# Kernel tuning notes

Hardware: AMD Instinct MI355X
Metric: run time of the kernel (lower is better)

## Reference

```python
import jax, jax.numpy as jnp
import numpy as np

T = 2_000_000  # timesteps


def setup_inputs() -> dict:
    key = jax.random.key(0)
    u = jax.random.normal(key, (T, 2), dtype=jnp.float32) * 10.0  # external forces per step
    x0 = jnp.zeros((4,), dtype=jnp.float32)  # [z1, v1, z2, v2]
    c = jnp.array([10.0, 10.0, 10.0], dtype=jnp.float32)   # trainable damping c1,c2,c3
    m = jnp.array([20.0, 10.0], dtype=jnp.float32)          # masses m1,m2 (frozen)
    k = jnp.array([2.0e3, 1.0e3, 5.0e3], dtype=jnp.float32) # stiffness k1,k2,k3 (frozen)
    dt = jnp.float32(0.002)
    return {"u": u, "x0": x0, "c": c, "m": m, "k": k, "dt": dt}


def reference(u, x0, c, m, k, dt):
    c1, c2, c3 = c[0], c[1], c[2]
    m1, m2 = m[0], m[1]
    k1, k2, k3 = k[0], k[1], k[2]

    def deriv(x, ut):
        # x = [z1, v1, z2, v2]; returns dx/dt = [v1, a1, v2, a2]
        z1, v1, z2, v2 = x[0], x[1], x[2], x[3]
        a1 = (ut[0] - (c1 + c2) * v1 + c2 * v2 - (k1 + k2) * z1 + k2 * z2) / m1
        a2 = (ut[1] - (c3 + c2) * v2 + c2 * v1 - (k3 + k2) * z2 + k2 * z1) / m2
        return jnp.stack([v1, a1, v2, a2])

    half = dt * 0.5

    def step(x, ut):
        s1 = deriv(x, ut)
        s2 = deriv(x + half * s1, ut)
        s3 = deriv(x + half * s2, ut)
        s4 = deriv(x + dt * s3, ut)
        xn = x + (dt / 6.0) * (s1 + 2.0 * s2 + 2.0 * s3 + s4)
        y = jnp.stack([xn[0], xn[2]])  # positions z1, z2 (matches cell output)
        return xn, y

    _, ys = jax.lax.scan(step, x0, u)
    return ys  # [T, 2]
```

## Files before the change

### kernel.cpp

```cpp
#include <hip/hip_runtime.h>

#define BLK 256
#define LS  32
#define SPB (BLK*LS)
#define STR (LS+1)

#define WC_M   0
#define WC_N   16
#define WC_SK  24
#define WC_GK  152
#define WC_TOT 280

#define WS_BAR_F32   1024
#define BAR_ARR_U32  0
#define BAR_FLAG_U32 272
#define BAR_BYTES    1152

typedef unsigned long long u64t;
union F2U { float2 f; u64t u; };

#define STEP4(Mx,Nx, s0,s1,s2,s3, ux,uy, n0,n1,n2,n3)                                              \
  n0 = fmaf(Mx[0],s0,  fmaf(Mx[1],s1,  fmaf(Mx[2],s2,  fmaf(Mx[3],s3,  fmaf(Nx[0],ux, Nx[1]*uy))))); \
  n1 = fmaf(Mx[4],s0,  fmaf(Mx[5],s1,  fmaf(Mx[6],s2,  fmaf(Mx[7],s3,  fmaf(Nx[2],ux, Nx[3]*uy))))); \
  n2 = fmaf(Mx[8],s0,  fmaf(Mx[9],s1,  fmaf(Mx[10],s2, fmaf(Mx[11],s3, fmaf(Nx[4],ux, Nx[5]*uy))))); \
  n3 = fmaf(Mx[12],s0, fmaf(Mx[13],s1, fmaf(Mx[14],s2, fmaf(Mx[15],s3, fmaf(Nx[6],ux, Nx[7]*uy)))));

__device__ __forceinline__ float4 aff_apply(const float* Mx, float4 l, float4 c) {
  float4 r;
  r.x = fmaf(Mx[0],l.x,  fmaf(Mx[1],l.y,  fmaf(Mx[2],l.z,  fmaf(Mx[3],l.w,  c.x))));
  r.y = fmaf(Mx[4],l.x,  fmaf(Mx[5],l.y,  fmaf(Mx[6],l.z,  fmaf(Mx[7],l.w,  c.y))));
  r.z = fmaf(Mx[8],l.x,  fmaf(Mx[9],l.y,  fmaf(Mx[10],l.z, fmaf(Mx[11],l.w, c.z))));
  r.w = fmaf(Mx[12],l.x, fmaf(Mx[13],l.y, fmaf(Mx[14],l.z, fmaf(Mx[15],l.w, c.w))));
  return r;
}

__device__ __forceinline__ float4 matvec(const float* Mx, float4 v) {
  return aff_apply(Mx, v, make_float4(0.f, 0.f, 0.f, 0.f));
}

__device__ __forceinline__ float4 shfl_up4(float4 v, int d) {
  return make_float4(__shfl_up(v.x, d, 64), __shfl_up(v.y, d, 64),
                     __shfl_up(v.z, d, 64), __shfl_up(v.w, d, 64));
}

__device__ __forceinline__ double mm_el(double x, double y, int i, int j) {
  double s = 0.0;
  #pragma unroll
  for (int l = 0; l < 4; ++l)
    s = fma(__shfl(x, 4*i + l, 64), __shfl(y, 4*l + j, 64), s);
  return s;
}

__device__ __forceinline__ void wave_setup(const float* __restrict__ cin,
                                           const float* __restrict__ min_,
                                           const float* __restrict__ kin,
                                           const float* __restrict__ dtin,
                                           float* C, int lane) {
  double c1 = cin[0], c2 = cin[1], c3 = cin[2];
  double m1 = min_[0], m2 = min_[1];
  double k1 = kin[0], k2 = kin[1], k3 = kin[2];
  double h  = dtin[0];
  const int i = (lane >> 2) & 3, j = lane & 3;

  double a;
  if (i == 0)      a = (j == 1) ? 1.0 : 0.0;
  else if (i == 2) a = (j == 3) ? 1.0 : 0.0;
  else if (i == 1) a = (j==0) ? -(k1+k2)/m1 : (j==1) ? -(c1+c2)/m1
                     : (j==2) ?  k2/m1      :  c2/m1;
  else             a = (j==0) ?  k2/m2      : (j==1) ?  c2/m2
                     : (j==2) ? -(k3+k2)/m2 : -(c3+c2)/m2;

  const double id = (i == j) ? 1.0 : 0.0;
  double q  = id + (h/4.0)*a;
  double t  = mm_el(a, q,  i, j);
  double r  = id + (h/3.0)*t;
  t         = mm_el(a, r,  i, j);
  double s_ = id + (h/2.0)*t;
  t         = mm_el(a, s_, i, j);
  double m  = id + h*t;
  if (lane < 16) C[WC_M + lane] = (float)m;

  {
    int e = lane & 7, ii = e >> 1, jp = e & 1, col = jp ? 3 : 1;
    double sv = __shfl(s_, 4*ii + col, 64);
    double nv = h * sv / (jp ? m2 : m1);
    if (lane < 8) C[WC_N + lane] = (float)nv;
  }

  double p = m;
  #pragma unroll
  for (int rr = 0; rr < 5; ++rr) p = mm_el(p, p, i, j);
  if (lane < 16) C[WC_SK + lane] = (float)p;
  #pragma unroll
  for (int k = 1; k < 8; ++k) {
    p = mm_el(p, p, i, j);
    if (lane < 16) C[WC_SK + 16*k + lane] = (float)p;
  }
  p = mm_el(p, p, i, j);
  if (lane < 16) C[WC_GK + lane] = (float)p;
  #pragma unroll
  for (int k = 1; k < 8; ++k) {
    p = mm_el(p, p, i, j);
    if (lane < 16) C[WC_GK + 16*k + lane] = (float)p;
  }
}

__device__ __forceinline__ float4 wave_scan(const float* SK, float4 b, int lane) {
  float4 cur = b;
  #pragma unroll
  for (int k = 0; k < 6; ++k) {
    int off = 1 << k;
    float4 l  = shfl_up4(cur, off);
    float4 nv = aff_apply(&SK[16*k], l, cur);
    if (lane >= off) cur = nv;
  }
  return cur;
}

__device__ __forceinline__ float4 cross_wave_excl(const float* SK, const float4* Wagg, int w) {
  float4 E = make_float4(0.f, 0.f, 0.f, 0.f);
  if (w > 0) {
    E = Wagg[0];
    for (int q = 1; q < w; ++q) E = aff_apply(&SK[16*6], E, Wagg[q]);
  }
  return E;
}

__launch_bounds__(BLK, 2)
__global__ void k_fused(const float4* __restrict__ u4,
                        const float* __restrict__ cc, const float* __restrict__ mmp,
                        const float* __restrict__ kp, const float* __restrict__ dtp,
                        float4* __restrict__ agg, unsigned* __restrict__ bar,
                        const float* __restrict__ x0in, float4* __restrict__ out4,
                        int T2, int nblk) {
  __shared__ float  uxp[BLK*STR];
  __shared__ float  uyp[BLK*STR];
  __shared__ float4 MA[256];
  __shared__ float4 MB[256];
  __shared__ float  C[WC_TOT];
  __shared__ float4 Wagg[4];
  const int tid   = threadIdx.x;
  const int bid   = blockIdx.x;
  const int lane  = tid & 63, w = tid >> 6;
  const int base2 = bid * SPB;

  if (tid < 64) wave_setup(cc, mmp, kp, dtp, C, tid);

  #pragma unroll
  for (int b = 0; b < 2; ++b) {
    float4 vbuf[8];
    #pragma unroll
    for (int q = 0; q < 8; ++q) {
      int idx4 = tid + (b*8 + q)*BLK;
      float4 v = make_float4(0.f, 0.f, 0.f, 0.f);
      if (base2 + 2*idx4 < T2) v = u4[(base2 >> 1) + idx4];
      vbuf[q] = v;
    }
    #pragma unroll
    for (int q = 0; q < 8; ++q) {
      int idx4 = tid + (b*8 + q)*BLK;
      int s0 = 2*idx4;
      int t0 = s0 >> 5, j0 = s0 & 31;
      int j1 = j0 + 1;
      uxp[t0*STR + j0] = vbuf[q].x;  uyp[t0*STR + j0] = vbuf[q].y;
      uxp[t0*STR + j1] = vbuf[q].z;  uyp[t0*STR + j1] = vbuf[q].w;
    }
  }
  __syncthreads();

  float Mm[16], Nn[8];
  #pragma unroll
  for (int i = 0; i < 16; ++i) Mm[i] = C[WC_M+i];
  #pragma unroll
  for (int i = 0; i < 8;  ++i) Nn[i] = C[WC_N+i];
  const float* SK = &C[WC_SK];
  const float* GK = &C[WC_GK];

  float b0 = 0.f, b1 = 0.f, b2 = 0.f, b3 = 0.f;
  #pragma unroll
  for (int j = 0; j < LS; ++j) {
    float ux = uxp[tid*STR + j], uy = uyp[tid*STR + j];
    float n0, n1, n2, n3;
    STEP4(Mm, Nn, b0, b1, b2, b3, ux, uy, n0, n1, n2, n3);
    b0 = n0; b1 = n1; b2 = n2; b3 = n3;
  }

  float4 incl = wave_scan(SK, make_float4(b0, b1, b2, b3), lane);
  if (lane == 63) Wagg[w] = incl;
  __syncthreads();

  if (tid == BLK-1) {
    float4 E = cross_wave_excl(SK, Wagg, 3);
    float4 t_ = matvec(&SK[16*6], E);
    F2U lo, hi;
    lo.f = make_float2(incl.x + t_.x, incl.y + t_.y);
    hi.f = make_float2(incl.z + t_.z, incl.w + t_.w);
    u64t* aggu = (u64t*)(agg + bid);
    __hip_atomic_store(aggu + 0, lo.u, __ATOMIC_RELAXED, __HIP_MEMORY_SCOPE_AGENT);
    __hip_atomic_store(aggu + 1, hi.u, __ATOMIC_RELAXED, __HIP_MEMORY_SCOPE_AGENT);
    asm volatile("s_waitcnt vmcnt(0)" ::: "memory");
    __hip_atomic_store(&bar[BAR_ARR_U32 + bid], 1u,
                       __ATOMIC_RELAXED, __HIP_MEMORY_SCOPE_AGENT);
  }

  if (bid == 0 && w == 3) {
    for (;;) {
      int ok = 1;
      #pragma unroll
      for (int it = 0; it < 4; ++it) {
        int i = lane + 64*it;
        unsigned v = __hip_atomic_load(&bar[BAR_ARR_U32 + i],
                                       __ATOMIC_RELAXED, __HIP_MEMORY_SCOPE_AGENT);
        ok &= (i >= nblk) | (v != 0u);
      }
      if (__all(ok)) break;
      __builtin_amdgcn_s_sleep(4);
    }
    if (lane == 63)
      __hip_atomic_store(&bar[BAR_FLAG_U32], 1u,
                         __ATOMIC_RELAXED, __HIP_MEMORY_SCOPE_AGENT);
  } else if (tid == BLK-1) {
    while (!__hip_atomic_load(&bar[BAR_FLAG_U32],
                              __ATOMIC_RELAXED, __HIP_MEMORY_SCOPE_AGENT))
      __builtin_amdgcn_s_sleep(8);
  }
  __syncthreads();

  const int n = nblk + 1;
  if (tid < n) MA[tid] = (tid == 0) ? make_float4(x0in[0], x0in[1], x0in[2], x0in[3])
                                    : agg[tid-1];
  __syncthreads();

  float4* Aa = MA; float4* Bb = MB;
  for (int k = 0; k < 8; ++k) {
    int off = 1 << k;
    if (off >= n) break;
    if (tid < n) {
      float4 v = Aa[tid];
      if (tid >= off) v = aff_apply(&GK[16*k], Aa[tid-off], v);
      Bb[tid] = v;
    }
    __syncthreads();
    float4* t = Aa; Aa = Bb; Bb = t;
  }

  float4 Xbs = Aa[bid];

  float4 E  = cross_wave_excl(SK, Wagg, w);
  float4 Xw = Xbs;
  if (w & 1) Xw = matvec(&SK[16*6], Xw);
  if (w & 2) Xw = matvec(&SK[16*7], Xw);
  Xw = make_float4(Xw.x + E.x, Xw.y + E.y, Xw.z + E.z, Xw.w + E.w);

  float4 ex = shfl_up4(incl, 1);
  if (lane == 0) ex = make_float4(0.f, 0.f, 0.f, 0.f);
  float4 v = Xw;
  #pragma unroll
  for (int k = 0; k < 6; ++k)
    if (lane & (1 << k)) v = matvec(&SK[16*k], v);
  float x0 = v.x + ex.x, x1 = v.y + ex.y, x2 = v.z + ex.z, x3 = v.w + ex.w;

  #pragma unroll
  for (int j = 0; j < LS; ++j) {
    float ux = uxp[tid*STR + j], uy = uyp[tid*STR + j];
    float n0, n1, n2, n3;
    STEP4(Mm, Nn, x0, x1, x2, x3, ux, uy, n0, n1, n2, n3);
    x0 = n0; x1 = n1; x2 = n2; x3 = n3;
    uxp[tid*STR + j] = x0;
    uyp[tid*STR + j] = x2;
  }
  __syncthreads();

  #pragma unroll
  for (int kk = 0; kk < SPB/2/BLK; ++kk) {
    int idx4 = tid + kk*BLK;
    int s0 = 2*idx4;
    if (base2 + s0 < T2) {
      int t0 = s0 >> 5, j0 = s0 & 31;
      int j1 = j0 + 1;
      out4[(base2 >> 1) + idx4] = make_float4(uxp[t0*STR + j0], uyp[t0*STR + j0],
                                              uxp[t0*STR + j1], uyp[t0*STR + j1]);
    }
  }
}

extern "C" void kernel_launch(void* const* d_in, const int* in_sizes, int n_in,
                              void* d_out, int out_size, void* d_ws, size_t ws_size,
                              hipStream_t stream) {
  const float4* u4  = (const float4*)d_in[0];
  const float*  x0  = (const float*)d_in[1];
  const float*  cc  = (const float*)d_in[2];
  const float*  mm  = (const float*)d_in[3];
  const float*  kk  = (const float*)d_in[4];
  const float*  dt  = (const float*)d_in[5];

  int T2   = in_sizes[0] / 2;
  int nblk = (T2 + SPB - 1) / SPB;

  float*    ws  = (float*)d_ws;
  float4*   agg = (float4*)ws;
  unsigned* bar = (unsigned*)(ws + WS_BAR_F32);

  hipMemsetAsync((void*)bar, 0, BAR_BYTES, stream);

  k_fused<<<nblk, BLK, 0, stream>>>(u4, cc, mm, kk, dt, agg, bar, x0,
                                    (float4*)d_out, T2, nblk);
}
```

Measured before the change: 93.08 us.

## Split fused scan kernel into three launches instead of a software grid barrier

Replaces the single persistent kernel, which used atomic flags and spin-waiting as a grid-wide barrier, with three kernels. The first computes per-block aggregates, the second is a single-block scan over those aggregates, and the third recomputes the states and writes the outputs. Per-thread inclusive scan results and constants are saved to workspace so the third pass can rebuild its prefix. This removes the spin-wait, the atomics and the memset. In exchange it adds two kernel launch gaps, a second read of u from global memory, and extra workspace traffic.

```diff
diff --git a/kernel.cpp b/kernel.cpp
--- a/kernel.cpp
+++ b/kernel.cpp
@@ -11,13 +11,10 @@
 #define WC_GK  152
 #define WC_TOT 280
 
-#define WS_BAR_F32   1024
-#define BAR_ARR_U32  0
-#define BAR_FLAG_U32 272
-#define BAR_BYTES    1152
-
-typedef unsigned long long u64t;
-union F2U { float2 f; u64t u; };
+#define WS_AGG_F32  0
+#define WS_XBS_F32  1024
+#define WS_C_F32    2048
+#define WS_INCL_F32 4096
 
 #define STEP4(Mx,Nx, s0,s1,s2,s3, ux,uy, n0,n1,n2,n3)                                              \
   n0 = fmaf(Mx[0],s0,  fmaf(Mx[1],s1,  fmaf(Mx[2],s2,  fmaf(Mx[3],s3,  fmaf(Nx[0],ux, Nx[1]*uy))))); \
@@ -126,17 +123,14 @@
   return E;
 }
 
-__launch_bounds__(BLK, 2)
-__global__ void k_fused(const float4* __restrict__ u4,
+__launch_bounds__(BLK)
+__global__ void k_pass1(const float4* __restrict__ u4,
                         const float* __restrict__ cc, const float* __restrict__ mmp,
                         const float* __restrict__ kp, const float* __restrict__ dtp,
-                        float4* __restrict__ agg, unsigned* __restrict__ bar,
-                        const float* __restrict__ x0in, float4* __restrict__ out4,
-                        int T2, int nblk) {
+                        float4* __restrict__ agg, float* __restrict__ wsc,
+                        float4* __restrict__ incl4, int T2) {
   __shared__ float  uxp[BLK*STR];
   __shared__ float  uyp[BLK*STR];
-  __shared__ float4 MA[256];
-  __shared__ float4 MB[256];
   __shared__ float  C[WC_TOT];
   __shared__ float4 Wagg[4];
   const int tid   = threadIdx.x;
@@ -161,12 +155,14 @@
       int idx4 = tid + (b*8 + q)*BLK;
       int s0 = 2*idx4;
       int t0 = s0 >> 5, j0 = s0 & 31;
-      int j1 = j0 + 1;
-      uxp[t0*STR + j0] = vbuf[q].x;  uyp[t0*STR + j0] = vbuf[q].y;
-      uxp[t0*STR + j1] = vbuf[q].z;  uyp[t0*STR + j1] = vbuf[q].w;
-    }
-  }
-  __syncthreads();
+      uxp[t0*STR + j0]   = vbuf[q].x;  uyp[t0*STR + j0]   = vbuf[q].y;
+      uxp[t0*STR + j0+1] = vbuf[q].z;  uyp[t0*STR + j0+1] = vbuf[q].w;
+    }
+  }
+  __syncthreads();
+
+  if (bid == 0)
+    for (int i = tid; i < WC_TOT; i += BLK) wsc[i] = C[i];
 
   float Mm[16], Nn[8];
   #pragma unroll
@@ -174,7 +170,6 @@
   #pragma unroll
   for (int i = 0; i < 8;  ++i) Nn[i] = C[WC_N+i];
   const float* SK = &C[WC_SK];
-  const float* GK = &C[WC_GK];
 
   float b0 = 0.f, b1 = 0.f, b2 = 0.f, b3 = 0.f;
   #pragma unroll
@@ -186,47 +181,28 @@
   }
 
   float4 incl = wave_scan(SK, make_float4(b0, b1, b2, b3), lane);
+  incl4[bid*BLK + tid] = incl;
   if (lane == 63) Wagg[w] = incl;
   __syncthreads();
 
   if (tid == BLK-1) {
-    float4 E = cross_wave_excl(SK, Wagg, 3);
+    float4 E  = cross_wave_excl(SK, Wagg, 3);
     float4 t_ = matvec(&SK[16*6], E);
-    F2U lo, hi;
-    lo.f = make_float2(incl.x + t_.x, incl.y + t_.y);
-    hi.f = make_float2(incl.z + t_.z, incl.w + t_.w);
-    u64t* aggu = (u64t*)(agg + bid);
-    __hip_atomic_store(aggu + 0, lo.u, __ATOMIC_RELAXED, __HIP_MEMORY_SCOPE_AGENT);
-    __hip_atomic_store(aggu + 1, hi.u, __ATOMIC_RELAXED, __HIP_MEMORY_SCOPE_AGENT);
-    asm volatile("s_waitcnt vmcnt(0)" ::: "memory");
-    __hip_atomic_store(&bar[BAR_ARR_U32 + bid], 1u,
-                       __ATOMIC_RELAXED, __HIP_MEMORY_SCOPE_AGENT);
-  }
-
-  if (bid == 0 && w == 3) {
-    for (;;) {
-      int ok = 1;
-      #pragma unroll
-      for (int it = 0; it < 4; ++it) {
-        int i = lane + 64*it;
-        unsigned v = __hip_atomic_load(&bar[BAR_ARR_U32 + i],
-                                       __ATOMIC_RELAXED, __HIP_MEMORY_SCOPE_AGENT);
-        ok &= (i >= nblk) | (v != 0u);
-      }
-      if (__all(ok)) break;
-      __builtin_amdgcn_s_sleep(4);
-    }
-    if (lane == 63)
-      __hip_atomic_store(&bar[BAR_FLAG_U32], 1u,
-                         __ATOMIC_RELAXED, __HIP_MEMORY_SCOPE_AGENT);
-  } else if (tid == BLK-1) {
-    while (!__hip_atomic_load(&bar[BAR_FLAG_U32],
-                              __ATOMIC_RELAXED, __HIP_MEMORY_SCOPE_AGENT))
-      __builtin_amdgcn_s_sleep(8);
-  }
-  __syncthreads();
-
+    agg[bid] = make_float4(incl.x + t_.x, incl.y + t_.y, incl.z + t_.z, incl.w + t_.w);
+  }
+}
+
+__launch_bounds__(BLK)
+__global__ void k_mid(const float4* __restrict__ agg, const float* __restrict__ wsc,
+                      const float* __restrict__ x0in, float4* __restrict__ xbs,
+                      int nblk) {
+  __shared__ float4 MA[256];
+  __shared__ float4 MB[256];
+  __shared__ float  GKs[128];
+  const int tid = threadIdx.x;
   const int n = nblk + 1;
+
+  if (tid < 128) GKs[tid] = wsc[WC_GK + tid];
   if (tid < n) MA[tid] = (tid == 0) ? make_float4(x0in[0], x0in[1], x0in[2], x0in[3])
                                     : agg[tid-1];
   __syncthreads();
@@ -237,23 +213,69 @@
     if (off >= n) break;
     if (tid < n) {
       float4 v = Aa[tid];
-      if (tid >= off) v = aff_apply(&GK[16*k], Aa[tid-off], v);
+      if (tid >= off) v = aff_apply(&GKs[16*k], Aa[tid-off], v);
       Bb[tid] = v;
     }
     __syncthreads();
     float4* t = Aa; Aa = Bb; Bb = t;
   }
-
-  float4 Xbs = Aa[bid];
-
-  float4 E  = cross_wave_excl(SK, Wagg, w);
-  float4 Xw = Xbs;
+  if (tid < n) xbs[tid] = Aa[tid];
+}
+
+__launch_bounds__(BLK)
+__global__ void k_pass3(const float4* __restrict__ u4,
+                        const float* __restrict__ wsc,
+                        const float4* __restrict__ incl4,
+                        const float4* __restrict__ xbs,
+                        float4* __restrict__ out4, int T2) {
+  __shared__ float  uxp[BLK*STR];
+  __shared__ float  uyp[BLK*STR];
+  __shared__ float  C[WC_TOT];
+  __shared__ float4 WaggS[4];
+  const int tid   = threadIdx.x;
+  const int bid   = blockIdx.x;
+  const int lane  = tid & 63, w = tid >> 6;
+  const int base2 = bid * SPB;
+  const int gid   = bid*BLK + tid;
+
+  for (int i = tid; i < WC_TOT; i += BLK) C[i] = wsc[i];
+  if (tid < 4) WaggS[tid] = incl4[bid*BLK + tid*64 + 63];
+  float4 ex = (lane == 0) ? make_float4(0.f, 0.f, 0.f, 0.f) : incl4[gid-1];
+
+  #pragma unroll
+  for (int b = 0; b < 2; ++b) {
+    float4 vbuf[8];
+    #pragma unroll
+    for (int q = 0; q < 8; ++q) {
+      int idx4 = tid + (b*8 + q)*BLK;
+      float4 v = make_float4(0.f, 0.f, 0.f, 0.f);
+      if (base2 + 2*idx4 < T2) v = u4[(base2 >> 1) + idx4];
+      vbuf[q] = v;
+    }
+    #pragma unroll
+    for (int q = 0; q < 8; ++q) {
+      int idx4 = tid + (b*8 + q)*BLK;
+      int s0 = 2*idx4;
+      int t0 = s0 >> 5, j0 = s0 & 31;
+      uxp[t0*STR + j0]   = vbuf[q].x;  uyp[t0*STR + j0]   = vbuf[q].y;
+      uxp[t0*STR + j0+1] = vbuf[q].z;  uyp[t0*STR + j0+1] = vbuf[q].w;
+    }
+  }
+  __syncthreads();
+
+  float Mm[16], Nn[8];
+  #pragma unroll
+  for (int i = 0; i < 16; ++i) Mm[i] = C[WC_M+i];
+  #pragma unroll
+  for (int i = 0; i < 8;  ++i) Nn[i] = C[WC_N+i];
+  const float* SK = &C[WC_SK];
+
+  float4 E  = cross_wave_excl(SK, WaggS, w);
+  float4 Xw = xbs[bid];
   if (w & 1) Xw = matvec(&SK[16*6], Xw);
   if (w & 2) Xw = matvec(&SK[16*7], Xw);
   Xw = make_float4(Xw.x + E.x, Xw.y + E.y, Xw.z + E.z, Xw.w + E.w);
 
-  float4 ex = shfl_up4(incl, 1);
-  if (lane == 0) ex = make_float4(0.f, 0.f, 0.f, 0.f);
   float4 v = Xw;
   #pragma unroll
   for (int k = 0; k < 6; ++k)
@@ -277,9 +299,8 @@
     int s0 = 2*idx4;
     if (base2 + s0 < T2) {
       int t0 = s0 >> 5, j0 = s0 & 31;
-      int j1 = j0 + 1;
-      out4[(base2 >> 1) + idx4] = make_float4(uxp[t0*STR + j0], uyp[t0*STR + j0],
-                                              uxp[t0*STR + j1], uyp[t0*STR + j1]);
+      out4[(base2 >> 1) + idx4] = make_float4(uxp[t0*STR + j0],   uyp[t0*STR + j0],
+                                              uxp[t0*STR + j0+1], uyp[t0*STR + j0+1]);
     }
   }
 }
@@ -297,12 +318,13 @@
   int T2   = in_sizes[0] / 2;
   int nblk = (T2 + SPB - 1) / SPB;
 
-  float*    ws  = (float*)d_ws;
-  float4*   agg = (float4*)ws;
-  unsigned* bar = (unsigned*)(ws + WS_BAR_F32);
-
-  hipMemsetAsync((void*)bar, 0, BAR_BYTES, stream);
-
-  k_fused<<<nblk, BLK, 0, stream>>>(u4, cc, mm, kk, dt, agg, bar, x0,
-                                    (float4*)d_out, T2, nblk);
-}
+  float*  ws    = (float*)d_ws;
+  float4* agg   = (float4*)(ws + WS_AGG_F32);
+  float4* xbs   = (float4*)(ws + WS_XBS_F32);
+  float*  wsc   = ws + WS_C_F32;
+  float4* incl4 = (float4*)(ws + WS_INCL_F32);
+
+  k_pass1<<<nblk, BLK, 0, stream>>>(u4, cc, mm, kk, dt, agg, wsc, incl4, T2);
+  k_mid  <<<1,    BLK, 0, stream>>>(agg, wsc, x0, xbs, nblk);
+  k_pass3<<<nblk, BLK, 0, stream>>>(u4, wsc, incl4, xbs, (float4*)d_out, T2);
+}
```

Result: no change. 93.16 us (+0.1%).
